# Performance work log

Hardware: AMD Instinct MI355X
Metric: run time of the kernel (lower is better)

The kernel has to match this reference:

```python
import jax, jax.numpy as jnp
import numpy as np

BATCH = 65536
INPUT_DIM = 256
FIELD_DIM = 32
OUTPUT_DIM = 30


def setup_inputs() -> dict:
    key = jax.random.key(0)
    k1, k2, k3 = jax.random.split(key, 3)
    x = jax.random.normal(k1, (BATCH, INPUT_DIM), dtype=jnp.float32)
    kernel = jax.random.normal(k2, (INPUT_DIM, OUTPUT_DIM), dtype=jnp.float32) * 0.1
    field_weight_matrix = jax.random.normal(k3, (FIELD_DIM, FIELD_DIM), dtype=jnp.float32) * 0.1
    # field_dict[i] = i % FIELD_DIM (matches init_kwargs)
    field_ids = (jnp.arange(INPUT_DIM) % FIELD_DIM).astype(jnp.int32)
    return {"x": x, "kernel": kernel, "field_weight_matrix": field_weight_matrix, "field_ids": field_ids}


def reference(x, kernel, field_weight_matrix, field_ids):
    # Pairwise factor weights: (k_i . k_j) for all i,j  -> [D, D]
    kk = kernel @ kernel.T
    # Field-weight gather: F[field[i], field[j]]  -> [D, D]
    fw = field_weight_matrix[field_ids[:, None], field_ids[None, :]]
    # Only i < j pairs, as in the original double loop
    M = jnp.triu(kk * fw, k=1)
    # out_b = sum_{i<j} x_bi * x_bj * M_ij
    out = jnp.einsum("bi,ij,bj->b", x, M, x)
    return out
```

## Files before the change

### kernel.cpp

```cpp
#include <hip/hip_runtime.h>
#include <stdint.h>
#include <stddef.h>

#define IDIM    256
#define FDIM    32
#define ODIM    30

typedef __attribute__((ext_vector_type(8))) short bf16x8;
typedef __attribute__((ext_vector_type(4))) float f32x4;

__device__ __forceinline__ short f2bf(float f) {
    union { float f; unsigned u; } v; v.f = f;
    unsigned r = v.u + 0x7FFFu + ((v.u >> 16) & 1u);
    return (short)(r >> 16);
}

__global__ void build_M(const float* __restrict__ K, const float* __restrict__ FW,
                        const int* __restrict__ FI, char* __restrict__ Mws) {
    const int i = blockIdx.x;
    const int j = threadIdx.x;
    float acc = 0.f;
    #pragma unroll
    for (int k = 0; k < ODIM; ++k) acc += K[i*ODIM + k] * K[j*ODIM + k];
    float m = 0.f;
    if (j > i) m = acc * FW[FI[i]*FDIM + FI[j]];
    const unsigned off = (unsigned)i*512u + (((unsigned)(2*j)) ^ ((unsigned)((i & 7) << 4)));
    *(short*)(Mws + off) = f2bf(m);
}

__global__ __launch_bounds__(512, 2)
void qform(const float* __restrict__ X, const char* __restrict__ Mws,
           float* __restrict__ out) {
    __shared__ char lds[131072];
    const int tid  = threadIdx.x;
    const int lane = tid & 63;
    const int wave = tid >> 6;
    const int wrow = blockIdx.x * 256 + wave * 32;

    #pragma unroll
    for (int it = 0; it < 16; ++it) {
        const char* g = Mws + it*8192 + tid*16;
        char*       l = lds + it*8192 + wave*1024;
        __builtin_amdgcn_global_load_lds(
            (const __attribute__((address_space(1))) unsigned int*)g,
            (__attribute__((address_space(3))) unsigned int*)l,
            16, 0, 0);
    }

    bf16x8 afrag[2][8];
    {
        const int arow = lane & 15;
        const int kgrp = (lane >> 4) * 8;
        #pragma unroll
        for (int s = 0; s < 2; ++s) {
            const float* xr = X + (size_t)(wrow + s*16 + arow) * IDIM + kgrp;
            #pragma unroll
            for (int tj = 0; tj < 8; ++tj) {
                float4 f0 = *(const float4*)(xr + tj*32);
                float4 f1 = *(const float4*)(xr + tj*32 + 4);
                bf16x8 a;
                a[0]=f2bf(f0.x); a[1]=f2bf(f0.y); a[2]=f2bf(f0.z); a[3]=f2bf(f0.w);
                a[4]=f2bf(f1.x); a[5]=f2bf(f1.y); a[6]=f2bf(f1.z); a[7]=f2bf(f1.w);
                afrag[s][tj] = a;
            }
        }
    }

    asm volatile("s_waitcnt vmcnt(0)" ::: "memory");
    __syncthreads();

    f32x4 acc[2][16];
    #pragma unroll
    for (int s = 0; s < 2; ++s)
        #pragma unroll
        for (int t = 0; t < 16; ++t)
            acc[s][t] = (f32x4){0.f, 0.f, 0.f, 0.f};

    const unsigned lrow512 = (unsigned)(lane & 15) * 512u;
    const unsigned grp16   = (unsigned)(lane >> 4) * 16u;
    const unsigned xorv    = (unsigned)(lane & 7) << 4;

    #pragma unroll
    for (int tj = 0; tj < 8; ++tj) {
        const unsigned jb = ((unsigned)(tj*64) + grp16) ^ xorv;
        const int timax = 2*tj + 1;
        #pragma unroll
        for (int ti = 0; ti <= timax && ti < 16; ++ti) {
            bf16x8 b = *(const bf16x8*)(lds + (unsigned)ti*8192u + lrow512 + jb);
            acc[0][ti] = __builtin_amdgcn_mfma_f32_16x16x32_bf16(afrag[0][tj], b, acc[0][ti], 0, 0, 0);
            acc[1][ti] = __builtin_amdgcn_mfma_f32_16x16x32_bf16(afrag[1][tj], b, acc[1][ti], 0, 0, 0);
        }
    }

    float psum[2][4] = {{0.f,0.f,0.f,0.f},{0.f,0.f,0.f,0.f}};
    const int g4 = (lane >> 4) * 4;
    #pragma unroll
    for (int ti = 0; ti < 16; ++ti) {
        const int col = ti*16 + (lane & 15);
        #pragma unroll
        for (int s = 0; s < 2; ++s) {
            const float* xc = X + (size_t)(wrow + s*16 + g4) * IDIM + col;
            #pragma unroll
            for (int r = 0; r < 4; ++r)
                psum[s][r] += xc[(size_t)r * IDIM] * acc[s][ti][r];
        }
    }

    #pragma unroll
    for (int s = 0; s < 2; ++s)
        #pragma unroll
        for (int r = 0; r < 4; ++r) {
            float v = psum[s][r];
            v += __shfl_xor(v, 1, 64);
            v += __shfl_xor(v, 2, 64);
            v += __shfl_xor(v, 4, 64);
            v += __shfl_xor(v, 8, 64);
            psum[s][r] = v;
        }

    if ((lane & 15) == 0) {
        #pragma unroll
        for (int s = 0; s < 2; ++s)
            #pragma unroll
            for (int r = 0; r < 4; ++r)
                out[wrow + s*16 + g4 + r] = psum[s][r];
    }
}

extern "C" void kernel_launch(void* const* d_in, const int* in_sizes, int n_in,
                              void* d_out, int out_size, void* d_ws, size_t ws_size,
                              hipStream_t stream) {
    const float* X  = (const float*)d_in[0];
    const float* K  = (const float*)d_in[1];
    const float* FW = (const float*)d_in[2];
    const int*   FI = (const int*)d_in[3];
    char* Mws = (char*)d_ws;

    build_M<<<dim3(256), dim3(256), 0, stream>>>(K, FW, FI, Mws);

    const int batch = in_sizes[0] / IDIM;
    qform<<<dim3(batch / 256), dim3(512), 0, stream>>>(X, Mws, (float*)d_out);
}
```

Before: 109.1 us.

## Fuse M construction into qform kernel with packed triangular LDS layout

Removes the separate build_M launch. Each block now builds the upper-triangular M tiles itself in LDS, computing K·Kᵀ with MFMA and applying the field-weight gather, using a packed triangular layout of only the needed tiles. This lowers LDS use so more blocks fit per CU (launch bounds 4). Each block now handles 128 rows, one 16-row strip per wave, and X loads are prefetched during the MFMA loop. The trade-off is that every block recomputes M redundantly and pays extra work before the main loop.

```diff
diff --git a/kernel.cpp b/kernel.cpp
--- a/kernel.cpp
+++ b/kernel.cpp
@@ -2,9 +2,7 @@
 #include <stdint.h>
 #include <stddef.h>
 
-#define IDIM    256
-#define FDIM    32
-#define ODIM    30
+#define IDIM 256
 
 typedef __attribute__((ext_vector_type(8))) short bf16x8;
 typedef __attribute__((ext_vector_type(4))) float f32x4;
@@ -15,115 +13,173 @@
     return (short)(r >> 16);
 }
 
-__global__ void build_M(const float* __restrict__ K, const float* __restrict__ FW,
-                        const int* __restrict__ FI, char* __restrict__ Mws) {
-    const int i = blockIdx.x;
-    const int j = threadIdx.x;
-    float acc = 0.f;
-    #pragma unroll
-    for (int k = 0; k < ODIM; ++k) acc += K[i*ODIM + k] * K[j*ODIM + k];
-    float m = 0.f;
-    if (j > i) m = acc * FW[FI[i]*FDIM + FI[j]];
-    const unsigned off = (unsigned)i*512u + (((unsigned)(2*j)) ^ ((unsigned)((i & 7) << 4)));
-    *(short*)(Mws + off) = f2bf(m);
-}
+#define FIOFF 73728
+#define FWOFF 74752
+#define LDSZ  78848
 
-__global__ __launch_bounds__(512, 2)
-void qform(const float* __restrict__ X, const char* __restrict__ Mws,
-           float* __restrict__ out) {
-    __shared__ char lds[131072];
+#define SWZ(r) ((((r) >> 1) & 3) << 4)
+
+__global__ __launch_bounds__(512, 4)
+void fused_qform(const float* __restrict__ X, const float* __restrict__ K,
+                 const float* __restrict__ FW, const int* __restrict__ FI,
+                 float* __restrict__ out) {
+    __shared__ char lds[LDSZ];
     const int tid  = threadIdx.x;
     const int lane = tid & 63;
     const int wave = tid >> 6;
-    const int wrow = blockIdx.x * 256 + wave * 32;
+    const int l15  = lane & 15;
+    const int g    = lane >> 4;
+    const int wrow = blockIdx.x * 128 + wave * 16;
 
-    #pragma unroll
-    for (int it = 0; it < 16; ++it) {
-        const char* g = Mws + it*8192 + tid*16;
-        char*       l = lds + it*8192 + wave*1024;
+    if (wave < 4) {
+        const char* src = (const char*)FW + wave * 1024 + lane * 16;
         __builtin_amdgcn_global_load_lds(
-            (const __attribute__((address_space(1))) unsigned int*)g,
-            (__attribute__((address_space(3))) unsigned int*)l,
+            (const __attribute__((address_space(1))) unsigned*)src,
+            (__attribute__((address_space(3))) unsigned*)(lds + FWOFF + wave * 1024),
+            16, 0, 0);
+    } else if (wave == 4) {
+        const char* src = (const char*)FI + lane * 16;
+        __builtin_amdgcn_global_load_lds(
+            (const __attribute__((address_space(1))) unsigned*)src,
+            (__attribute__((address_space(3))) unsigned*)(lds + FIOFF),
             16, 0, 0);
     }
 
-    bf16x8 afrag[2][8];
+    const int kbase = g * 8;
+    const int tb1 = wave;
+    const int tb2 = 15 - wave;
+    bf16x8 fragA[16], fragB1, fragB2;
+    #pragma unroll
+    for (int t = 0; t < 16; ++t) {
+        const float* kr = K + (16 * t + l15) * 30 + kbase;
+        bf16x8 f;
+        #pragma unroll
+        for (int e = 0; e < 8; ++e) {
+            float v = (kbase + e < 30) ? kr[e] : 0.f;
+            f[e] = f2bf(v);
+        }
+        fragA[t] = f;
+    }
     {
-        const int arow = lane & 15;
-        const int kgrp = (lane >> 4) * 8;
+        const float* kr = K + (16 * tb1 + l15) * 30 + kbase;
+        bf16x8 f;
         #pragma unroll
-        for (int s = 0; s < 2; ++s) {
-            const float* xr = X + (size_t)(wrow + s*16 + arow) * IDIM + kgrp;
-            #pragma unroll
-            for (int tj = 0; tj < 8; ++tj) {
-                float4 f0 = *(const float4*)(xr + tj*32);
-                float4 f1 = *(const float4*)(xr + tj*32 + 4);
-                bf16x8 a;
-                a[0]=f2bf(f0.x); a[1]=f2bf(f0.y); a[2]=f2bf(f0.z); a[3]=f2bf(f0.w);
-                a[4]=f2bf(f1.x); a[5]=f2bf(f1.y); a[6]=f2bf(f1.z); a[7]=f2bf(f1.w);
-                afrag[s][tj] = a;
+        for (int e = 0; e < 8; ++e) { float v = (kbase + e < 30) ? kr[e] : 0.f; f[e] = f2bf(v); }
+        fragB1 = f;
+    }
+    {
+        const float* kr = K + (16 * tb2 + l15) * 30 + kbase;
+        bf16x8 f;
+        #pragma unroll
+        for (int e = 0; e < 8; ++e) { float v = (kbase + e < 30) ? kr[e] : 0.f; f[e] = f2bf(v); }
+        fragB2 = f;
+    }
+    const int fij1 = FI[16 * tb1 + l15];
+    const int fij2 = FI[16 * tb2 + l15];
+
+    {
+        const int ht = wave;
+        const int r  = (lane >> 2) & 15;
+        const int a  = lane & 3;
+        const int zb = ((ht * (ht + 1) + (2 * ht + 1)) << 10) + r * 64 + ((a * 8) ^ SWZ(r));
+        *(unsigned long long*)(lds + zb) = 0ull;
+    }
+
+    asm volatile("s_waitcnt vmcnt(0) lgkmcnt(0)" ::: "memory");
+    __builtin_amdgcn_s_barrier();
+    asm volatile("" ::: "memory");
+
+    const float* xrow = X + (size_t)(wrow + l15) * IDIM + kbase;
+    float4 xa[8], xb[8];
+    xa[0] = *(const float4*)(xrow + 0 * 32);
+    xb[0] = *(const float4*)(xrow + 0 * 32 + 4);
+
+    const f32x4 kz = (f32x4){0.f, 0.f, 0.f, 0.f};
+    const int* ldsFI = (const int*)(lds + FIOFF);
+    const float* ldsFW = (const float*)(lds + FWOFF);
+
+#define BUILD_TILE(ta, tb, fb, fij) do {                                          \
+        f32x4 kk = __builtin_amdgcn_mfma_f32_16x16x32_bf16(fragA[ta], fb, kz, 0, 0, 0); \
+        const int tjm = (tb) >> 1;                                                \
+        const int mb  = ((tjm * (tjm + 1) + (ta)) << 10);                         \
+        const int jb0 = (((tb) & 1) << 5) + 2 * l15;                              \
+        const int j   = 16 * (tb) + l15;                                          \
+        _Pragma("unroll")                                                         \
+        for (int q = 0; q < 4; ++q) {                                             \
+            const int i15 = g * 4 + q;                                            \
+            const int i   = 16 * (ta) + i15;                                      \
+            const float fw = ldsFW[ldsFI[16 * (ta) + i15] * 32 + (fij)];          \
+            const float val = (j > i) ? kk[q] * fw : 0.f;                         \
+            *(short*)(lds + mb + i15 * 64 + (jb0 ^ SWZ(i15))) = f2bf(val);        \
+        }                                                                         \
+    } while (0)
+
+    #pragma unroll
+    for (int ta = 0; ta < 16; ++ta) {
+        if (ta <= tb1) BUILD_TILE(ta, tb1, fragB1, fij1);
+    }
+    #pragma unroll
+    for (int ta = 0; ta < 16; ++ta) {
+        if (ta <= tb2) BUILD_TILE(ta, tb2, fragB2, fij2);
+    }
+#undef BUILD_TILE
+
+    asm volatile("s_waitcnt lgkmcnt(0)" ::: "memory");
+    __builtin_amdgcn_s_barrier();
+    asm volatile("" ::: "memory");
+
+    f32x4 acc[16];
+    #pragma unroll
+    for (int t = 0; t < 16; ++t) acc[t] = kz;
+
+    xa[1] = *(const float4*)(xrow + 1 * 32);
+    xb[1] = *(const float4*)(xrow + 1 * 32 + 4);
+    xa[2] = *(const float4*)(xrow + 2 * 32);
+    xb[2] = *(const float4*)(xrow + 2 * 32 + 4);
+
+    const unsigned laneoff = (unsigned)l15 * 64u + (unsigned)((g * 16) ^ SWZ(l15));
+
+    #pragma unroll
+    for (int tj = 0; tj < 8; ++tj) {
+        if (tj < 5) {
+            xa[tj + 3] = *(const float4*)(xrow + (tj + 3) * 32);
+            xb[tj + 3] = *(const float4*)(xrow + (tj + 3) * 32 + 4);
+        }
+        const float4 fa = xa[tj], fb = xb[tj];
+        bf16x8 af;
+        af[0] = f2bf(fa.x); af[1] = f2bf(fa.y); af[2] = f2bf(fa.z); af[3] = f2bf(fa.w);
+        af[4] = f2bf(fb.x); af[5] = f2bf(fb.y); af[6] = f2bf(fb.z); af[7] = f2bf(fb.w);
+        #pragma unroll
+        for (int ti = 0; ti < 16; ++ti) {
+            if (ti <= 2 * tj + 1) {
+                const bf16x8 b = *(const bf16x8*)(lds + ((tj * (tj + 1) + ti) << 10) + laneoff);
+                acc[ti] = __builtin_amdgcn_mfma_f32_16x16x32_bf16(af, b, acc[ti], 0, 0, 0);
             }
         }
     }
 
-    asm volatile("s_waitcnt vmcnt(0)" ::: "memory");
-    __syncthreads();
-
-    f32x4 acc[2][16];
-    #pragma unroll
-    for (int s = 0; s < 2; ++s)
-        #pragma unroll
-        for (int t = 0; t < 16; ++t)
-            acc[s][t] = (f32x4){0.f, 0.f, 0.f, 0.f};
-
-    const unsigned lrow512 = (unsigned)(lane & 15) * 512u;
-    const unsigned grp16   = (unsigned)(lane >> 4) * 16u;
-    const unsigned xorv    = (unsigned)(lane & 7) << 4;
-
-    #pragma unroll
-    for (int tj = 0; tj < 8; ++tj) {
-        const unsigned jb = ((unsigned)(tj*64) + grp16) ^ xorv;
-        const int timax = 2*tj + 1;
-        #pragma unroll
-        for (int ti = 0; ti <= timax && ti < 16; ++ti) {
-            bf16x8 b = *(const bf16x8*)(lds + (unsigned)ti*8192u + lrow512 + jb);
-            acc[0][ti] = __builtin_amdgcn_mfma_f32_16x16x32_bf16(afrag[0][tj], b, acc[0][ti], 0, 0, 0);
-            acc[1][ti] = __builtin_amdgcn_mfma_f32_16x16x32_bf16(afrag[1][tj], b, acc[1][ti], 0, 0, 0);
-        }
-    }
-
-    float psum[2][4] = {{0.f,0.f,0.f,0.f},{0.f,0.f,0.f,0.f}};
-    const int g4 = (lane >> 4) * 4;
+    float psum[4] = {0.f, 0.f, 0.f, 0.f};
+    const float* xm = X + (size_t)(wrow + g * 4) * IDIM + l15;
     #pragma unroll
     for (int ti = 0; ti < 16; ++ti) {
-        const int col = ti*16 + (lane & 15);
         #pragma unroll
-        for (int s = 0; s < 2; ++s) {
-            const float* xc = X + (size_t)(wrow + s*16 + g4) * IDIM + col;
-            #pragma unroll
-            for (int r = 0; r < 4; ++r)
-                psum[s][r] += xc[(size_t)r * IDIM] * acc[s][ti][r];
-        }
+        for (int q = 0; q < 4; ++q)
+            psum[q] += xm[(size_t)q * IDIM + ti * 16] * acc[ti][q];
     }
 
     #pragma unroll
-    for (int s = 0; s < 2; ++s)
+    for (int q = 0; q < 4; ++q) {
+        float v = psum[q];
+        v += __shfl_xor(v, 1, 64);
+        v += __shfl_xor(v, 2, 64);
+        v += __shfl_xor(v, 4, 64);
+        v += __shfl_xor(v, 8, 64);
+        psum[q] = v;
+    }
+    if (l15 == 0) {
         #pragma unroll
-        for (int r = 0; r < 4; ++r) {
-            float v = psum[s][r];
-            v += __shfl_xor(v, 1, 64);
-            v += __shfl_xor(v, 2, 64);
-            v += __shfl_xor(v, 4, 64);
-            v += __shfl_xor(v, 8, 64);
-            psum[s][r] = v;
-        }
-
-    if ((lane & 15) == 0) {
-        #pragma unroll
-        for (int s = 0; s < 2; ++s)
-            #pragma unroll
-            for (int r = 0; r < 4; ++r)
-                out[wrow + s*16 + g4 + r] = psum[s][r];
+        for (int q = 0; q < 4; ++q)
+            out[wrow + g * 4 + q] = psum[q];
     }
 }
 
@@ -134,10 +190,6 @@
     const float* K  = (const float*)d_in[1];
     const float* FW = (const float*)d_in[2];
     const int*   FI = (const int*)d_in[3];
-    char* Mws = (char*)d_ws;
-
-    build_M<<<dim3(256), dim3(256), 0, stream>>>(K, FW, FI, Mws);
-
     const int batch = in_sizes[0] / IDIM;
-    qform<<<dim3(batch / 256), dim3(512), 0, stream>>>(X, Mws, (float*)d_out);
+    fused_qform<<<dim3(batch / 128), dim3(512), 0, stream>>>(X, K, FW, FI, (float*)d_out);
 }
```

New measurement: 139.3 us. 1.28x slower.
